# Performance work log

Hardware: AMD Instinct MI355X
Metric: run time of the kernel (lower is better)

The kernel has to match this reference:

```python
import jax, jax.numpy as jnp
import numpy as np

B, S, D = 1, 2048, 2048
N_HEADS, N_KV_HEADS = 32, 8
HEAD_DIM = D // N_HEADS  # 64
N_REP = N_HEADS // N_KV_HEADS  # 4


def setup_inputs() -> dict:
    key = jax.random.key(0)
    ks = jax.random.split(key, 6)
    x = jax.random.normal(ks[0], (B, S, D), dtype=jnp.float32)
    # weights stored as [in, out] so projection is x @ W
    wq = jax.random.normal(ks[1], (D, N_HEADS * HEAD_DIM), dtype=jnp.float32) * 0.02
    wk = jax.random.normal(ks[2], (D, N_KV_HEADS * HEAD_DIM), dtype=jnp.float32) * 0.02
    wv = jax.random.normal(ks[3], (D, N_KV_HEADS * HEAD_DIM), dtype=jnp.float32) * 0.02
    wo = jax.random.normal(ks[4], (N_HEADS * HEAD_DIM, D), dtype=jnp.float32) * 0.02
    # RoPE tables: freqs_cis has shape (seqlen, head_dim//2)
    theta = 10000.0
    inv_freq = 1.0 / (theta ** (jnp.arange(0, HEAD_DIM, 2, dtype=jnp.float32) / HEAD_DIM))
    angles = jnp.arange(S, dtype=jnp.float32)[:, None] * inv_freq[None, :]  # [S, hd/2]
    freqs_cos = jnp.cos(angles)
    freqs_sin = jnp.sin(angles)
    # causal additive mask, broadcast to [b, h, q, k]
    mask = jnp.triu(jnp.full((S, S), -jnp.inf, dtype=jnp.float32), k=1)[None, None]
    return {"x": x, "wq": wq, "wk": wk, "wv": wv, "wo": wo,
            "freqs_cos": freqs_cos, "freqs_sin": freqs_sin, "mask": mask}


def _apply_rope(t, cos, sin):
    # t: [B, S, H, head_dim]; pairs (t[...,2i], t[...,2i+1]) form complex numbers
    tr = t[..., 0::2]
    ti = t[..., 1::2]
    c = cos[None, :, None, :]
    s = sin[None, :, None, :]
    out_r = tr * c - ti * s
    out_i = tr * s + ti * c
    return jnp.stack([out_r, out_i], axis=-1).reshape(t.shape)


def reference(x, wq, wk, wv, wo, freqs_cos, freqs_sin, mask):
    bsz, seqlen, _ = x.shape
    xq = (x @ wq).reshape(bsz, seqlen, N_HEADS, HEAD_DIM)
    xk = (x @ wk).reshape(bsz, seqlen, N_KV_HEADS, HEAD_DIM)
    xv = (x @ wv).reshape(bsz, seqlen, N_KV_HEADS, HEAD_DIM)
    xq = _apply_rope(xq, freqs_cos, freqs_sin)
    xk = _apply_rope(xk, freqs_cos, freqs_sin)
    # repeat_kv (GQA expansion): [b,s,kvh,d] -> [b,s,h,d]
    keys = jnp.repeat(xk, N_REP, axis=2)
    values = jnp.repeat(xv, N_REP, axis=2)
    scale = 1.0 / np.sqrt(HEAD_DIM)
    # scores: [b, h, q, k]
    scores = jnp.einsum('bqhd,bkhd->bhqk', xq, keys) * scale
    scores = scores + mask
    probs = jax.nn.softmax(scores.astype(jnp.float32), axis=-1).astype(x.dtype)
    out = jnp.einsum('bhqk,bkhd->bqhd', probs, values)
    out = out.reshape(bsz, seqlen, N_HEADS * HEAD_DIM)
    return out @ wo
```

## Files before the change

### kernel.cpp

```cpp
#include <hip/hip_runtime.h>
#include <hip/hip_bf16.h>

#define S_LEN 2048
#define D_MODEL 2048
#define N_HEADS 32
#define N_KV 8
#define HEAD_DIM 64
#define KV_DIM (N_KV * HEAD_DIM)
#define QKV_N (D_MODEL + 2 * KV_DIM)

typedef __bf16 bf16_t;
typedef __attribute__((ext_vector_type(8))) __bf16 bf16x8;
typedef __attribute__((ext_vector_type(4))) float f32x4;
typedef __attribute__((ext_vector_type(16))) float f32x16;
typedef __attribute__((ext_vector_type(4))) unsigned int uint4v;
typedef __attribute__((ext_vector_type(2))) unsigned int uint2v;

__device__ __forceinline__ void gload_lds16(const void* g, void* l) {
    __builtin_amdgcn_global_load_lds(
        (const __attribute__((address_space(1))) unsigned char*)g,
        (__attribute__((address_space(3))) unsigned char*)l,
        16, 0, 0);
}

__global__ __launch_bounds__(256) void transpose_convert(const float* __restrict__ src,
                                                         __hip_bfloat16* __restrict__ dst,
                                                         int R, int C) {
    __shared__ float tile[32][33];
    const int bx = blockIdx.x * 32;
    const int by = blockIdx.y * 32;
    const int tx = threadIdx.x;
    const int ty = threadIdx.y;
#pragma unroll
    for (int i = 0; i < 32; i += 8)
        tile[ty + i][tx] = src[(size_t)(by + ty + i) * C + bx + tx];
    __syncthreads();
#pragma unroll
    for (int i = 0; i < 32; i += 8)
        dst[(size_t)(bx + ty + i) * R + by + tx] = __float2bfloat16(tile[tx][ty + i]);
}

__global__ __launch_bounds__(256) void convert_bf16(const float* __restrict__ src,
                                                    __hip_bfloat16* __restrict__ dst) {
    const int i = (blockIdx.x * 256 + threadIdx.x) * 8;
    const float4 a = *reinterpret_cast<const float4*>(src + i);
    const float4 b = *reinterpret_cast<const float4*>(src + i + 4);
    bf16x8 r;
    r[0] = (__bf16)a.x; r[1] = (__bf16)a.y; r[2] = (__bf16)a.z; r[3] = (__bf16)a.w;
    r[4] = (__bf16)b.x; r[5] = (__bf16)b.y; r[6] = (__bf16)b.z; r[7] = (__bf16)b.w;
    *reinterpret_cast<bf16x8*>(dst + i) = r;
}

__global__ __launch_bounds__(256) void rope_qk(__hip_bfloat16* __restrict__ t,
                                               const float* __restrict__ cos_t,
                                               const float* __restrict__ sin_t) {
    const int idx = blockIdx.x * blockDim.x + threadIdx.x;
    const int i = idx & 31;
    const int hh = (idx >> 5) % (N_HEADS + N_KV);
    const int s = idx / (32 * (N_HEADS + N_KV));
    const float c = cos_t[s * 32 + i];
    const float sn = sin_t[s * 32 + i];
    int col; float scale;
    if (hh < N_HEADS) { col = hh * HEAD_DIM + 2 * i; scale = 0.125f * 1.44269504f; }
    else { col = D_MODEL + (hh - N_HEADS) * HEAD_DIM + 2 * i; scale = 1.0f; }
    __hip_bfloat16* p = &t[(size_t)s * QKV_N + col];
    const float re = __bfloat162float(p[0]);
    const float im = __bfloat162float(p[1]);
    p[0] = __float2bfloat16((re * c - im * sn) * scale);
    p[1] = __float2bfloat16((re * sn + im * c) * scale);
}

__global__ __launch_bounds__(256) void transpose_v(const __hip_bfloat16* __restrict__ QKV,
                                                   __hip_bfloat16* __restrict__ Vt) {
    __shared__ __align__(16) __bf16 tile[64][72];
    const int s0 = blockIdx.x * 64;
    const int hkv = blockIdx.y;
    const int tid = threadIdx.x;
    {
        const int r = tid >> 2;
        const int c0 = (tid & 3) * 16;
        const __hip_bfloat16* src = QKV + (size_t)(s0 + r) * QKV_N + D_MODEL + KV_DIM + hkv * HEAD_DIM + c0;
        *reinterpret_cast<bf16x8*>(&tile[r][c0]) = *reinterpret_cast<const bf16x8*>(src);
        *reinterpret_cast<bf16x8*>(&tile[r][c0 + 8]) = *reinterpret_cast<const bf16x8*>(src + 8);
    }
    __syncthreads();
    {
        const int d = tid >> 2;
        const int sc = (tid & 3) * 16;
        bf16x8 o0, o1;
#pragma unroll
        for (int j = 0; j < 8; ++j) { o0[j] = tile[sc + j][d]; o1[j] = tile[sc + 8 + j][d]; }
        __hip_bfloat16* dst = Vt + (size_t)(hkv * HEAD_DIM + d) * S_LEN + s0 + sc;
        *reinterpret_cast<bf16x8*>(dst) = o0;
        *reinterpret_cast<bf16x8*>(dst + 8) = o1;
    }
}

__device__ inline void storeC(__hip_bfloat16* p, float v) { *p = __float2bfloat16(v); }
__device__ inline void storeC(float* p, float v) { *p = v; }

template <typename OutT>
__global__ __launch_bounds__(256) void gemm_bt(const __hip_bfloat16* __restrict__ A,
                                               const __hip_bfloat16* __restrict__ Bt,
                                               OutT* __restrict__ C,
                                               int M, int N, int K) {
    __shared__ __align__(16) __bf16 As[2][128 * 32];
    __shared__ __align__(16) __bf16 Bs[2][128 * 32];
    const int tid = threadIdx.x;
    const int w = tid >> 6, l = tid & 63;
    const int wr = w >> 1, wc = w & 1;
    const int l4 = l >> 4, l15 = l & 15;
    const int bm = blockIdx.y * 128, bn = blockIdx.x * 128;

    f32x4 acc[4][4];
#pragma unroll
    for (int i = 0; i < 4; ++i)
#pragma unroll
        for (int j = 0; j < 4; ++j) acc[i][j] = (f32x4){0.f, 0.f, 0.f, 0.f};

    const int r0 = tid >> 2;
    const int cc0 = tid & 3;

    auto stage = [&](int buf, int k0) {
#pragma unroll
        for (int p = 0; p < 2; ++p) {
            const int row = p * 64 + r0;
            const int cs = cc0 ^ (row & 3);
            gload_lds16(&A[(size_t)(bm + row) * K + k0 + cs * 8], &As[buf][(p * 256 + tid) * 8]);
            gload_lds16(&Bt[(size_t)(bn + row) * K + k0 + cs * 8], &Bs[buf][(p * 256 + tid) * 8]);
        }
    };

    const int nk = K >> 5;
    stage(0, 0);
    asm volatile("s_waitcnt vmcnt(0)" ::: "memory");
    __builtin_amdgcn_s_barrier();

#pragma unroll 2
    for (int kt = 0; kt < nk; ++kt) {
        const int cur = kt & 1;
        if (kt + 1 < nk) stage(cur ^ 1, (kt + 1) * 32);
        bf16x8 a[4], b[4];
#pragma unroll
        for (int mi = 0; mi < 4; ++mi) {
            const int rr = wr * 64 + mi * 16 + l15;
            a[mi] = *reinterpret_cast<const bf16x8*>(&As[cur][rr * 32 + ((l4 ^ (rr & 3))) * 8]);
        }
#pragma unroll
        for (int ni = 0; ni < 4; ++ni) {
            const int rr = wc * 64 + ni * 16 + l15;
            b[ni] = *reinterpret_cast<const bf16x8*>(&Bs[cur][rr * 32 + ((l4 ^ (rr & 3))) * 8]);
        }
#pragma unroll
        for (int mi = 0; mi < 4; ++mi)
#pragma unroll
            for (int ni = 0; ni < 4; ++ni)
                acc[mi][ni] = __builtin_amdgcn_mfma_f32_16x16x32_bf16(a[mi], b[ni], acc[mi][ni], 0, 0, 0);
        asm volatile("s_waitcnt vmcnt(0)" ::: "memory");
        __builtin_amdgcn_s_barrier();
    }
#pragma unroll
    for (int mi = 0; mi < 4; ++mi)
#pragma unroll
        for (int ni = 0; ni < 4; ++ni)
#pragma unroll
            for (int r = 0; r < 4; ++r) {
                const int row = bm + wr * 64 + mi * 16 + l4 * 4 + r;
                const int col = bn + wc * 64 + ni * 16 + l15;
                storeC(&C[(size_t)row * N + col], acc[mi][ni][r]);
            }
}

__device__ __forceinline__ unsigned cvtpk_bf16(float lo, float hi) {
    unsigned w;
    asm("v_cvt_pk_bf16_f32 %0, %1, %2" : "=v"(w) : "v"(lo), "v"(hi));
    return w;
}
template <int R0>
__device__ __forceinline__ bf16x8 build_pfrag(const f32x16& s, int hi) {
    const unsigned A0 = cvtpk_bf16(s[R0 + 0], s[R0 + 1]);
    const unsigned A1 = cvtpk_bf16(s[R0 + 2], s[R0 + 3]);
    const unsigned B0 = cvtpk_bf16(s[R0 + 4], s[R0 + 5]);
    const unsigned B1 = cvtpk_bf16(s[R0 + 6], s[R0 + 7]);
    const unsigned pA0 = __shfl_xor(A0, 32, 64);
    const unsigned pA1 = __shfl_xor(A1, 32, 64);
    const unsigned pB0 = __shfl_xor(B0, 32, 64);
    const unsigned pB1 = __shfl_xor(B1, 32, 64);
    uint4v u;
    u[0] = hi ? pB0 : A0;
    u[1] = hi ? pB1 : A1;
    u[2] = hi ? B0 : pA0;
    u[3] = hi ? B1 : pA1;
    return __builtin_bit_cast(bf16x8, u);
}

__global__ __launch_bounds__(512) void attn_kernel(const __hip_bfloat16* __restrict__ QKV,
                                                   const __hip_bfloat16* __restrict__ Vt,
                                                   __hip_bfloat16* __restrict__ O,
                                                   float* __restrict__ Opart,
                                                   float* __restrict__ ms,
                                                   int split) {
    const int h = blockIdx.y;
    const int hkv = h >> 2;
    int qc = 0, sl = 0, gbase = 0, ns = 1;
    if (!split) {
        qc = 7 - (int)blockIdx.x;
    } else {
        const int x = (int)blockIdx.x;
        int cum = 0;
#pragma unroll
        for (int q = 0; q < 8; ++q) {
            const int n = (q + 2) >> 1;
            if (x >= cum && x < cum + n) { qc = q; sl = x - cum; gbase = cum; }
            cum += n;
        }
        ns = (qc + 2) >> 1;
    }
    const int ntf = 4 * (qc + 1);
    const int t0 = split ? sl * 8 : 0;
    const int t1 = split ? min(t0 + 8, ntf) : ntf;

    const int tid = threadIdx.x;
    const int w = tid >> 6, l = tid & 63;
    const int lq = l & 31, hi = l >> 5;
    const int q0w = qc * 256 + w * 32;
    const int qlane = q0w + lq;

    __shared__ __align__(16) __bf16 Ks[2][64 * 64];
    __shared__ __align__(16) __bf16 Vs[2][64 * 64];

    const __hip_bfloat16* Kg = QKV + D_MODEL + hkv * HEAD_DIM;
    const __hip_bfloat16* Vg = Vt + (size_t)hkv * HEAD_DIM * S_LEN;

    auto stage = [&](int buf, int kv0) {
        const int chunk = tid;
        const int r = chunk >> 3;
        const int cs = (chunk & 7) ^ (r & 7);
        gload_lds16(&Kg[(size_t)(kv0 + r) * QKV_N + cs * 8], &Ks[buf][chunk * 8]);
        gload_lds16(&Vg[(size_t)r * S_LEN + kv0 + cs * 8], &Vs[buf][chunk * 8]);
    };

    bf16x8 qf[4];
#pragma unroll
    for (int f = 0; f < 4; ++f)
        qf[f] = *reinterpret_cast<const bf16x8*>(
            &QKV[(size_t)qlane * QKV_N + h * HEAD_DIM + 16 * f + 8 * hi]);

    f32x16 o0, o1;
#pragma unroll
    for (int r = 0; r < 16; ++r) { o0[r] = 0.f; o1[r] = 0.f; }
    float m_run = -__builtin_inff(), s_run = 0.f;

    stage(0, t0 * 64);

#pragma unroll 1
    for (int t = t0; t < t1; ++t) {
        __syncthreads();
        if (t + 1 < t1) stage((t + 1 - t0) & 1, (t + 1) * 64);
        const int kv0 = t * 64;
        if (kv0 <= q0w + 31) {
            const __bf16* Kb = Ks[(t - t0) & 1];
            const __bf16* Vb = Vs[(t - t0) & 1];

            f32x16 s0, s1;
#pragma unroll
            for (int r = 0; r < 16; ++r) { s0[r] = 0.f; s1[r] = 0.f; }
#pragma unroll
            for (int f = 0; f < 4; ++f) {
                const int rr0 = lq;
                const int rr1 = 32 + lq;
                const bf16x8 ka0 = *reinterpret_cast<const bf16x8*>(
                    &Kb[rr0 * 64 + (((2 * f + hi) ^ (rr0 & 7))) * 8]);
                const bf16x8 ka1 = *reinterpret_cast<const bf16x8*>(
                    &Kb[rr1 * 64 + (((2 * f + hi) ^ (rr1 & 7))) * 8]);
                s0 = __builtin_amdgcn_mfma_f32_32x32x16_bf16(ka0, qf[f], s0, 0, 0, 0);
                s1 = __builtin_amdgcn_mfma_f32_32x32x16_bf16(ka1, qf[f], s1, 0, 0, 0);
            }
            if (kv0 + 63 > q0w) {
#pragma unroll
                for (int r = 0; r < 16; ++r) {
                    const int kvb = (r & 3) + 8 * (r >> 2) + 4 * hi;
                    if (kv0 + kvb > qlane) s0[r] = -__builtin_inff();
                    if (kv0 + 32 + kvb > qlane) s1[r] = -__builtin_inff();
                }
            }
            float ta = fmaxf(s0[0], s1[0]), tb = fmaxf(s0[1], s1[1]);
            float tc = fmaxf(s0[2], s1[2]), td = fmaxf(s0[3], s1[3]);
#pragma unroll
            for (int r = 4; r < 16; r += 4) {
                ta = fmaxf(ta, fmaxf(s0[r], s1[r]));
                tb = fmaxf(tb, fmaxf(s0[r + 1], s1[r + 1]));
                tc = fmaxf(tc, fmaxf(s0[r + 2], s1[r + 2]));
                td = fmaxf(td, fmaxf(s0[r + 3], s1[r + 3]));
            }
            float m_row = fmaxf(fmaxf(ta, tb), fmaxf(tc, td));
            m_row = fmaxf(m_row, __shfl_xor(m_row, 32, 64));

            if (!__all(m_row <= m_run + 8.0f)) {
                const float mnew = fmaxf(m_run, m_row);
                const float corr = exp2f(m_run - mnew);
                m_run = mnew;
                s_run *= corr;
#pragma unroll
                for (int r = 0; r < 16; ++r) { o0[r] *= corr; o1[r] *= corr; }
            }
#pragma unroll
            for (int r = 0; r < 16; ++r) {
                s0[r] = exp2f(s0[r] - m_run);
                s1[r] = exp2f(s1[r] - m_run);
            }
            float ua = s0[0] + s1[0], ub = s0[1] + s1[1];
            float uc = s0[2] + s1[2], ud = s0[3] + s1[3];
#pragma unroll
            for (int r = 4; r < 16; r += 4) {
                ua += s0[r] + s1[r];
                ub += s0[r + 1] + s1[r + 1];
                uc += s0[r + 2] + s1[r + 2];
                ud += s0[r + 3] + s1[r + 3];
            }
            float rs = (ua + ub) + (uc + ud);
            rs += __shfl_xor(rs, 32, 64);
            s_run += rs;

            bf16x8 pa[4];
            pa[0] = build_pfrag<0>(s0, hi);
            pa[1] = build_pfrag<8>(s0, hi);
            pa[2] = build_pfrag<0>(s1, hi);
            pa[3] = build_pfrag<8>(s1, hi);

#pragma unroll
            for (int ks = 0; ks < 4; ++ks) {
                const int rv0 = lq;
                const int rv1 = 32 + lq;
                const bf16x8 va0 = *reinterpret_cast<const bf16x8*>(
                    &Vb[rv0 * 64 + (((2 * ks + hi) ^ (rv0 & 7))) * 8]);
                const bf16x8 va1 = *reinterpret_cast<const bf16x8*>(
                    &Vb[rv1 * 64 + (((2 * ks + hi) ^ (rv1 & 7))) * 8]);
                o0 = __builtin_amdgcn_mfma_f32_32x32x16_bf16(va0, pa[ks], o0, 0, 0, 0);
                o1 = __builtin_amdgcn_mfma_f32_32x32x16_bf16(va1, pa[ks], o1, 0, 0, 0);
            }
        }
    }

    if (ns == 1) {
        const float inv = 1.0f / s_run;
        __hip_bfloat16* orow = O + (size_t)qlane * D_MODEL + h * HEAD_DIM;
#pragma unroll
        for (int rr = 0; rr < 4; ++rr) {
            {
                uint2v u;
                u[0] = cvtpk_bf16(o0[4 * rr] * inv, o0[4 * rr + 1] * inv);
                u[1] = cvtpk_bf16(o0[4 * rr + 2] * inv, o0[4 * rr + 3] * inv);
                *reinterpret_cast<uint2v*>(orow + 8 * rr + 4 * hi) = u;
            }
            {
                uint2v u;
                u[0] = cvtpk_bf16(o1[4 * rr] * inv, o1[4 * rr + 1] * inv);
                u[1] = cvtpk_bf16(o1[4 * rr + 2] * inv, o1[4 * rr + 3] * inv);
                *reinterpret_cast<uint2v*>(orow + 32 + 8 * rr + 4 * hi) = u;
            }
        }
    } else {
        const int g = h * 20 + gbase + sl;
        const int row = w * 32 + lq;
        const size_t base = ((size_t)g * 256 + row) * 64;
#pragma unroll
        for (int rr = 0; rr < 4; ++rr) {
            f32x4 v0, v1;
#pragma unroll
            for (int j = 0; j < 4; ++j) { v0[j] = o0[4 * rr + j]; v1[j] = o1[4 * rr + j]; }
            *reinterpret_cast<f32x4*>(&Opart[base + 8 * rr + 4 * hi]) = v0;
            *reinterpret_cast<f32x4*>(&Opart[base + 32 + 8 * rr + 4 * hi]) = v1;
        }
        if (hi == 0) {
            const size_t mi = (size_t)g * 256 + row;
            ms[mi * 2] = m_run;
            ms[mi * 2 + 1] = s_run;
        }
    }
}

__device__ __constant__ int kCum[8] = {0, 1, 2, 4, 6, 9, 12, 16};

__global__ __launch_bounds__(256) void attn_merge(const float* __restrict__ Opart,
                                                  const float* __restrict__ ms,
                                                  __hip_bfloat16* __restrict__ O) {
    const int qc = 2 + blockIdx.x;
    const int h = blockIdx.z;
    const int tid = threadIdx.x;
    const int row = blockIdx.y * 32 + (tid >> 3);
    const int dv0 = (tid & 7) * 8;
    const int ns = (qc + 2) >> 1;
    const int g0 = h * 20 + kCum[qc];

    float mv[4], sv[4];
    float M = -__builtin_inff();
#pragma unroll
    for (int s = 0; s < 4; ++s) {
        if (s < ns) {
            const size_t mi = (size_t)(g0 + s) * 256 + row;
            mv[s] = ms[mi * 2];
            sv[s] = ms[mi * 2 + 1];
            M = fmaxf(M, mv[s]);
        }
    }
    float S = 0.f;
    float acc[8];
#pragma unroll
    for (int j = 0; j < 8; ++j) acc[j] = 0.f;
#pragma unroll
    for (int s = 0; s < 4; ++s) {
        if (s < ns) {
            const float wgt = exp2f(mv[s] - M);
            S += wgt * sv[s];
            const float* p = &Opart[((size_t)(g0 + s) * 256 + row) * 64 + dv0];
            const float4 a = *reinterpret_cast<const float4*>(p);
            const float4 b = *reinterpret_cast<const float4*>(p + 4);
            acc[0] += wgt * a.x; acc[1] += wgt * a.y; acc[2] += wgt * a.z; acc[3] += wgt * a.w;
            acc[4] += wgt * b.x; acc[5] += wgt * b.y; acc[6] += wgt * b.z; acc[7] += wgt * b.w;
        }
    }
    const float inv = 1.0f / S;
    uint4v u;
    u[0] = cvtpk_bf16(acc[0] * inv, acc[1] * inv);
    u[1] = cvtpk_bf16(acc[2] * inv, acc[3] * inv);
    u[2] = cvtpk_bf16(acc[4] * inv, acc[5] * inv);
    u[3] = cvtpk_bf16(acc[6] * inv, acc[7] * inv);
    *reinterpret_cast<uint4v*>(&O[(size_t)(qc * 256 + row) * D_MODEL + h * HEAD_DIM + dv0]) = u;
}

extern "C" void kernel_launch(void* const* d_in, const int* in_sizes, int n_in,
                              void* d_out, int out_size, void* d_ws, size_t ws_size,
                              hipStream_t stream) {
    const float* x  = (const float*)d_in[0];
    const float* wq = (const float*)d_in[1];
    const float* wk = (const float*)d_in[2];
    const float* wv = (const float*)d_in[3];
    const float* wo = (const float*)d_in[4];
    const float* fc = (const float*)d_in[5];
    const float* fs = (const float*)d_in[6];
    float* out = (float*)d_out;

    char* ws = (char*)d_ws;
    __hip_bfloat16* wqkvT = (__hip_bfloat16*)(ws);
    __hip_bfloat16* woT   = (__hip_bfloat16*)(ws + (12u << 20));
    __hip_bfloat16* attnb = (__hip_bfloat16*)(ws + (20u << 20));
    __hip_bfloat16* xb    = (__hip_bfloat16*)(ws + (28u << 20));
    __hip_bfloat16* QKV   = (__hip_bfloat16*)(ws + (36u << 20));
    __hip_bfloat16* Vt    = (__hip_bfloat16*)(ws + (48u << 20));
    float*          msb   = (float*)(ws + (50u << 20));
    float*          Opart = (float*)(ws + (53u << 20));

    const int split = (ws_size >= (96ull << 20)) ? 1 : 0;

    const dim3 tb(32, 8);
    transpose_convert<<<dim3(D_MODEL / 32, D_MODEL / 32), tb, 0, stream>>>(wq, wqkvT, D_MODEL, D_MODEL);
    transpose_convert<<<dim3(KV_DIM / 32, D_MODEL / 32), tb, 0, stream>>>(wk, wqkvT + (size_t)D_MODEL * D_MODEL, D_MODEL, KV_DIM);
    transpose_convert<<<dim3(KV_DIM / 32, D_MODEL / 32), tb, 0, stream>>>(wv, wqkvT + (size_t)(D_MODEL + KV_DIM) * D_MODEL, D_MODEL, KV_DIM);
    transpose_convert<<<dim3(D_MODEL / 32, D_MODEL / 32), tb, 0, stream>>>(wo, woT, D_MODEL, D_MODEL);
    convert_bf16<<<(S_LEN * D_MODEL) / (256 * 8), 256, 0, stream>>>(x, xb);

    gemm_bt<__hip_bfloat16><<<dim3(QKV_N / 128, S_LEN / 128), 256, 0, stream>>>(xb, wqkvT, QKV, S_LEN, QKV_N, D_MODEL);

    rope_qk<<<(S_LEN * (N_HEADS + N_KV) * 32) / 256, 256, 0, stream>>>(QKV, fc, fs);

    transpose_v<<<dim3(S_LEN / 64, N_KV), 256, 0, stream>>>(QKV, Vt);

    if (split) {
        attn_kernel<<<dim3(20, N_HEADS), 512, 0, stream>>>(QKV, Vt, attnb, Opart, msb, 1);
        attn_merge<<<dim3(6, 8, N_HEADS), 256, 0, stream>>>(Opart, msb, attnb);
    } else {
        attn_kernel<<<dim3(8, N_HEADS), 512, 0, stream>>>(QKV, Vt, attnb, Opart, msb, 0);
    }

    gemm_bt<float><<<dim3(D_MODEL / 128, S_LEN / 128), 256, 0, stream>>>(attnb, woT, out, S_LEN, D_MODEL, D_MODEL);

    (void)in_sizes; (void)n_in; (void)out_size;
}
```

Baseline: 176.1 us.

## Triple-buffer GEMM loads, raise MFMA priority, store attention partials in bf16

```diff
diff --git a/kernel.cpp b/kernel.cpp
--- a/kernel.cpp
+++ b/kernel.cpp
@@ -104,8 +104,8 @@
                                                const __hip_bfloat16* __restrict__ Bt,
                                                OutT* __restrict__ C,
                                                int M, int N, int K) {
-    __shared__ __align__(16) __bf16 As[2][128 * 32];
-    __shared__ __align__(16) __bf16 Bs[2][128 * 32];
+    __shared__ __align__(16) __bf16 As[3][128 * 32];
+    __shared__ __align__(16) __bf16 Bs[3][128 * 32];
     const int tid = threadIdx.x;
     const int w = tid >> 6, l = tid & 63;
     const int wr = w >> 1, wc = w & 1;
@@ -133,13 +133,14 @@
 
     const int nk = K >> 5;
     stage(0, 0);
-    asm volatile("s_waitcnt vmcnt(0)" ::: "memory");
+    stage(1, 32);
+    asm volatile("s_waitcnt vmcnt(4)" ::: "memory");
     __builtin_amdgcn_s_barrier();
 
-#pragma unroll 2
+    int cur = 0;
+#pragma unroll 1
     for (int kt = 0; kt < nk; ++kt) {
-        const int cur = kt & 1;
-        if (kt + 1 < nk) stage(cur ^ 1, (kt + 1) * 32);
+        if (kt + 2 < nk) stage(cur == 0 ? 2 : cur - 1, (kt + 2) * 32);
         bf16x8 a[4], b[4];
 #pragma unroll
         for (int mi = 0; mi < 4; ++mi) {
@@ -156,8 +157,12 @@
 #pragma unroll
             for (int ni = 0; ni < 4; ++ni)
                 acc[mi][ni] = __builtin_amdgcn_mfma_f32_16x16x32_bf16(a[mi], b[ni], acc[mi][ni], 0, 0, 0);
-        asm volatile("s_waitcnt vmcnt(0)" ::: "memory");
-        __builtin_amdgcn_s_barrier();
+        if (kt + 1 < nk) {
+            if (kt + 2 < nk) asm volatile("s_waitcnt vmcnt(4)" ::: "memory");
+            else             asm volatile("s_waitcnt vmcnt(0)" ::: "memory");
+            __builtin_amdgcn_s_barrier();
+        }
+        cur = (cur == 2) ? 0 : cur + 1;
     }
 #pragma unroll
     for (int mi = 0; mi < 4; ++mi)
@@ -197,7 +202,7 @@
 __global__ __launch_bounds__(512) void attn_kernel(const __hip_bfloat16* __restrict__ QKV,
                                                    const __hip_bfloat16* __restrict__ Vt,
                                                    __hip_bfloat16* __restrict__ O,
-                                                   float* __restrict__ Opart,
+                                                   __hip_bfloat16* __restrict__ Opart,
                                                    float* __restrict__ ms,
                                                    int split) {
     const int h = blockIdx.y;
@@ -265,6 +270,7 @@
             f32x16 s0, s1;
 #pragma unroll
             for (int r = 0; r < 16; ++r) { s0[r] = 0.f; s1[r] = 0.f; }
+            __builtin_amdgcn_s_setprio(1);
 #pragma unroll
             for (int f = 0; f < 4; ++f) {
                 const int rr0 = lq;
@@ -276,6 +282,7 @@
                 s0 = __builtin_amdgcn_mfma_f32_32x32x16_bf16(ka0, qf[f], s0, 0, 0, 0);
                 s1 = __builtin_amdgcn_mfma_f32_32x32x16_bf16(ka1, qf[f], s1, 0, 0, 0);
             }
+            __builtin_amdgcn_s_setprio(0);
             if (kv0 + 63 > q0w) {
 #pragma unroll
                 for (int r = 0; r < 16; ++r) {
@@ -328,6 +335,7 @@
             pa[2] = build_pfrag<0>(s1, hi);
             pa[3] = build_pfrag<8>(s1, hi);
 
+            __builtin_amdgcn_s_setprio(1);
 #pragma unroll
             for (int ks = 0; ks < 4; ++ks) {
                 const int rv0 = lq;
@@ -339,6 +347,7 @@
                 o0 = __builtin_amdgcn_mfma_f32_32x32x16_bf16(va0, pa[ks], o0, 0, 0, 0);
                 o1 = __builtin_amdgcn_mfma_f32_32x32x16_bf16(va1, pa[ks], o1, 0, 0, 0);
             }
+            __builtin_amdgcn_s_setprio(0);
         }
     }
 
@@ -363,14 +372,21 @@
     } else {
         const int g = h * 20 + gbase + sl;
         const int row = w * 32 + lq;
-        const size_t base = ((size_t)g * 256 + row) * 64;
+        __hip_bfloat16* pb = Opart + ((size_t)g * 256 + row) * 64;
 #pragma unroll
         for (int rr = 0; rr < 4; ++rr) {
-            f32x4 v0, v1;
-#pragma unroll
-            for (int j = 0; j < 4; ++j) { v0[j] = o0[4 * rr + j]; v1[j] = o1[4 * rr + j]; }
-            *reinterpret_cast<f32x4*>(&Opart[base + 8 * rr + 4 * hi]) = v0;
-            *reinterpret_cast<f32x4*>(&Opart[base + 32 + 8 * rr + 4 * hi]) = v1;
+            {
+                uint2v u;
+                u[0] = cvtpk_bf16(o0[4 * rr], o0[4 * rr + 1]);
+                u[1] = cvtpk_bf16(o0[4 * rr + 2], o0[4 * rr + 3]);
+                *reinterpret_cast<uint2v*>(pb + 8 * rr + 4 * hi) = u;
+            }
+            {
+                uint2v u;
+                u[0] = cvtpk_bf16(o1[4 * rr], o1[4 * rr + 1]);
+                u[1] = cvtpk_bf16(o1[4 * rr + 2], o1[4 * rr + 3]);
+                *reinterpret_cast<uint2v*>(pb + 32 + 8 * rr + 4 * hi) = u;
+            }
         }
         if (hi == 0) {
             const size_t mi = (size_t)g * 256 + row;
@@ -382,7 +398,7 @@
 
 __device__ __constant__ int kCum[8] = {0, 1, 2, 4, 6, 9, 12, 16};
 
-__global__ __launch_bounds__(256) void attn_merge(const float* __restrict__ Opart,
+__global__ __launch_bounds__(256) void attn_merge(const __hip_bfloat16* __restrict__ Opart,
                                                   const float* __restrict__ ms,
                                                   __hip_bfloat16* __restrict__ O) {
     const int qc = 2 + blockIdx.x;
@@ -413,11 +429,10 @@
         if (s < ns) {
             const float wgt = exp2f(mv[s] - M);
             S += wgt * sv[s];
-            const float* p = &Opart[((size_t)(g0 + s) * 256 + row) * 64 + dv0];
-            const float4 a = *reinterpret_cast<const float4*>(p);
-            const float4 b = *reinterpret_cast<const float4*>(p + 4);
-            acc[0] += wgt * a.x; acc[1] += wgt * a.y; acc[2] += wgt * a.z; acc[3] += wgt * a.w;
-            acc[4] += wgt * b.x; acc[5] += wgt * b.y; acc[6] += wgt * b.z; acc[7] += wgt * b.w;
+            const bf16x8 v = *reinterpret_cast<const bf16x8*>(
+                &Opart[((size_t)(g0 + s) * 256 + row) * 64 + dv0]);
+#pragma unroll
+            for (int j = 0; j < 8; ++j) acc[j] += wgt * (float)v[j];
         }
     }
     const float inv = 1.0f / S;
@@ -449,9 +464,9 @@
     __hip_bfloat16* QKV   = (__hip_bfloat16*)(ws + (36u << 20));
     __hip_bfloat16* Vt    = (__hip_bfloat16*)(ws + (48u << 20));
     float*          msb   = (float*)(ws + (50u << 20));
-    float*          Opart = (float*)(ws + (53u << 20));
-
-    const int split = (ws_size >= (96ull << 20)) ? 1 : 0;
+    __hip_bfloat16* Opart = (__hip_bfloat16*)(ws + (53u << 20));
+
+    const int split = (ws_size >= (80ull << 20)) ? 1 : 0;
 
     const dim3 tb(32, 8);
     transpose_convert<<<dim3(D_MODEL / 32, D_MODEL / 32), tb, 0, stream>>>(wq, wqkvT, D_MODEL, D_MODEL);
```

Measured after the change: 184.3 us. +4.7%, slower.
